# Kernel optimization log

Measured on AMD Instinct MI355X. Metric: run time of the kernel, lower is better.

The kernel has to match this reference:

```python
import jax, jax.numpy as jnp
import numpy as np

V, C, D = 4, 64, 64
LH, LW, FH, FW = 64, 96, 256, 384
MIN_DEPTH, MAX_DEPTH, MIN_UNC = 0.5, 10.0, 0.01


def conv2d(x, w, b=None, groups=1, pad=0):
    y = jax.lax.conv_general_dilated(x, w, (1, 1), [(pad, pad), (pad, pad)],
                                     feature_group_count=groups,
                                     dimension_numbers=('NCHW', 'OIHW', 'NCHW'))
    return y if b is None else y + b[None, :, None, None]


def group_norm(x, g, b, groups=8, eps=1e-5):
    N, Ch, H, W = x.shape
    xr = x.reshape(N, groups, Ch // groups, H, W)
    m = xr.mean((2, 3, 4), keepdims=True)
    v = ((xr - m) ** 2).mean((2, 3, 4), keepdims=True)
    xr = (xr - m) / jnp.sqrt(v + eps)
    return xr.reshape(N, Ch, H, W) * g[None, :, None, None] + b[None, :, None, None]


def ds_block(x, dw, pw_w, pw_b, gn_g, gn_b):
    # in_channels == out_channels everywhere here -> identity skip
    y = conv2d(x, dw, None, groups=x.shape[1], pad=1)
    y = conv2d(y, pw_w, pw_b)
    y = jax.nn.gelu(group_norm(y, gn_g, gn_b), approximate=False)
    return y + x


def resize_bilinear(x, oh, ow):
    # bilinear, align_corners=True, x: [N,C,H,W]
    N, Ch, H, W = x.shape
    ys = jnp.linspace(0.0, H - 1.0, oh)
    xs = jnp.linspace(0.0, W - 1.0, ow)
    y0 = jnp.clip(jnp.floor(ys).astype(jnp.int32), 0, H - 1)
    x0 = jnp.clip(jnp.floor(xs).astype(jnp.int32), 0, W - 1)
    y1 = jnp.minimum(y0 + 1, H - 1)
    x1 = jnp.minimum(x0 + 1, W - 1)
    wy = (ys - y0)[None, None, :, None]
    wx = (xs - x0)[None, None, None, :]
    r0 = x[:, :, y0, :]
    r1 = x[:, :, y1, :]
    a = r0[:, :, :, x0]; b = r0[:, :, :, x1]
    c = r1[:, :, :, x0]; d = r1[:, :, :, x1]
    return a * (1 - wy) * (1 - wx) + b * (1 - wy) * wx + c * wy * (1 - wx) + d * wy * wx


def grid_sample(img, grid):
    # bilinear, padding_mode='zeros', align_corners=True
    B, Ch, H, W = img.shape
    gx = (grid[..., 0] + 1.0) * 0.5 * (W - 1)
    gy = (grid[..., 1] + 1.0) * 0.5 * (H - 1)
    x0f = jnp.floor(gx); y0f = jnp.floor(gy)
    wx = gx - x0f; wy = gy - y0f
    def gather(xf, yf):
        valid = (xf >= 0) & (xf <= W - 1) & (yf >= 0) & (yf <= H - 1)
        xi = jnp.clip(xf, 0, W - 1).astype(jnp.int32)
        yi = jnp.clip(yf, 0, H - 1).astype(jnp.int32)
        v = jax.vmap(lambda im, yy, xx: im[:, yy, xx])(img, yi, xi)  # [B,C,Hg,Wg]
        return v * valid.astype(img.dtype)[:, None]
    return (gather(x0f, y0f) * ((1 - wx) * (1 - wy))[:, None]
            + gather(x0f + 1, y0f) * (wx * (1 - wy))[:, None]
            + gather(x0f, y0f + 1) * ((1 - wx) * wy)[:, None]
            + gather(x0f + 1, y0f + 1) * (wx * wy)[:, None])


def warp_volume(src_feats, inv_bins, K_ref, E_ref, K_src, W2C_src, H, W):
    # src_feats [B,C,H,W]; K_ref [3,3]; E_ref [4,4]; K_src [B,3,3]; W2C_src [B,4,4]
    B, Ch = src_feats.shape[:2]
    Dn = inv_bins.shape[0]
    depth_bins = 1.0 / inv_bins
    scale = jnp.array([W, H, 1.0], src_feats.dtype)
    Kr = K_ref * scale[:, None]
    Ks = K_src * scale[None, :, None]
    gy, gx = jnp.meshgrid(jnp.arange(H, dtype=src_feats.dtype),
                          jnp.arange(W, dtype=src_feats.dtype), indexing='ij')
    homog = jnp.stack([gx, gy, jnp.ones_like(gx)], 0).reshape(3, -1)          # [3,N]
    rays = jnp.linalg.inv(Kr) @ homog                                          # [3,N]
    ref_pts = rays[:, None, :] * depth_bins[None, :, None]                     # [3,D,N]
    world = jnp.einsum('ij,jdn->idn', E_ref[:3, :3], ref_pts) + E_ref[:3, 3][:, None, None]
    spts = jnp.einsum('bij,jdn->bidn', W2C_src[:, :3, :3], world) + W2C_src[:, :3, 3][:, :, None, None]
    proj = jnp.einsum('bij,bjdn->bidn', Ks, spts)                              # [B,3,D,N]
    xy = proj[:, :2] / jnp.maximum(proj[:, 2:3], 1e-6)
    xy = xy.reshape(B, 2, Dn, H, W)
    gxn = 2.0 * xy[:, 0] / max(W - 1, 1) - 1.0
    gyn = 2.0 * xy[:, 1] / max(H - 1, 1) - 1.0
    grid = jnp.stack([gxn, gyn], -1).reshape(B, Dn * H, W, 2)
    sz = proj[:, 2].reshape(B, Dn, H, W)
    vis = ((sz > 1e-6) & (xy[:, 0] >= 0) & (xy[:, 0] <= W - 1)
           & (xy[:, 1] >= 0) & (xy[:, 1] <= H - 1)).astype(src_feats.dtype)
    warped = grid_sample(src_feats, grid).reshape(B, Ch, Dn, H, W) * vis[:, None]
    return warped, vis


def _forward(lowres_features, fullres_features, images, intrinsics, extrinsics,
             dp_w, dp_b, cr_dw, cr_pw_w, cr_pw_b, cr_gn_g, cr_gn_b,
             fr_conv_w, fr_conv_b, fr_dw, fr_pw_w, fr_pw_b, fr_gn_g, fr_gn_b,
             res_w, res_b, conf_w, conf_b):
    nv, _, lh, lw = lowres_features.shape
    fh, fw = fullres_features.shape[-2:]
    imgs_r = resize_bilinear(images, fh, fw)
    inv_bins = jnp.linspace(1.0 / MAX_DEPTH, 1.0 / MIN_DEPTH, D).astype(lowres_features.dtype)
    w2c = jnp.linalg.inv(extrinsics)
    interval = (1.0 / MIN_DEPTH - 1.0 / MAX_DEPTH) / max(D - 1, 1)
    bins4 = inv_bins[None, :, None, None]
    depths, uncs, confs = [], [], []
    for r in range(nv):
        sidx = np.array([i for i in range(nv) if i != r])
        ref_feat = lowres_features[r]                       # [C,lh,lw]
        warped, vis = warp_volume(lowres_features[sidx], inv_bins,
                                  intrinsics[r], extrinsics[r],
                                  intrinsics[sidx], w2c[sidx], lh, lw)
        dot = jnp.einsum('chw,bcdhw->bdhw', ref_feat, warped)
        nr = jnp.sqrt((ref_feat ** 2).sum(0))               # [h,w]
        nw = jnp.sqrt((warped ** 2).sum(1))                 # [b,d,h,w]
        cos = dot / (jnp.maximum(nr, 1e-8) * jnp.maximum(nw, 1e-8))
        cost = (1.0 - cos) * vis + (1.0 - vis)
        agg = ((cost * vis).sum(0) / jnp.maximum(vis.sum(0), 1.0))[None]  # [1,D,h,w]
        rc = agg
        for i in range(2):
            rc = ds_block(rc, cr_dw[i], cr_pw_w[i], cr_pw_b[i], cr_gn_g[i], cr_gn_b[i])
        refined_cost = agg + rc
        logits = conv2d(ref_feat[None], dp_w, dp_b) - refined_cost
        prob = jax.nn.softmax(logits, axis=1)
        inv_low = (prob * bins4).sum(1, keepdims=True)
        var = (prob * (bins4 - inv_low) ** 2).sum(1, keepdims=True)
        inv_unc_low = jnp.maximum(jnp.sqrt(var), 1e-6)
        pdf_max = prob.max(axis=1, keepdims=True)
        inv_full = resize_bilinear(inv_low, fh, fw)
        inv_unc_full = resize_bilinear(inv_unc_low, fh, fw)
        pdf_max_full = resize_bilinear(pdf_max, fh, fw)
        y = jax.nn.gelu(conv2d(jnp.concatenate([fullres_features[r:r + 1], imgs_r[r:r + 1]], 1),
                               fr_conv_w, fr_conv_b, pad=1), approximate=False)
        for i in range(2):
            y = ds_block(y, fr_dw[i], fr_pw_w[i], fr_pw_b[i], fr_gn_g[i], fr_gn_b[i])
        resid = jnp.tanh(conv2d(y, res_w, res_b)) * interval
        inv_depth = jnp.clip(inv_full + resid, 1.0 / MAX_DEPTH, 1.0 / MIN_DEPTH)
        depth = 1.0 / inv_depth
        unc = jnp.maximum(inv_unc_full / jnp.maximum(inv_depth ** 2, 1e-6), MIN_UNC)
        conf = jax.nn.sigmoid(conv2d(y, conf_w, conf_b)) * pdf_max_full / (1.0 + inv_unc_full / max(interval, 1e-6))
        depths.append(depth); uncs.append(unc); confs.append(conf)
    return (jnp.concatenate(depths, 0), jnp.concatenate(uncs, 0), jnp.concatenate(confs, 0))


def setup_inputs() -> dict:
    key = jax.random.key(0)
    ks = jax.random.split(key, 16)
    f = jnp.float32
    lowres_features = jax.random.normal(ks[0], (V, C, LH, LW), f)
    fullres_features = jax.random.normal(ks[1], (V, C, FH, FW), f)
    images = jax.random.uniform(ks[2], (V, 3, FH, FW), dtype=f)
    # normalized pinhole intrinsics (module scales rows by width/height)
    K = np.array([[0.8, 0.0, 0.5], [0.0, 0.8, 0.5], [0.0, 0.0, 1.0]], np.float32)
    intrinsics = jnp.asarray(np.tile(K[None], (V, 1, 1)))
    # camera-to-world extrinsics: small y-rotations, 0.2m baseline steps
    angles = [0.0, 0.05, -0.05, 0.1]
    ext = np.tile(np.eye(4, dtype=np.float32)[None], (V, 1, 1))
    for v in range(V):
        a = angles[v]
        ext[v, :3, :3] = np.array([[np.cos(a), 0, np.sin(a)], [0, 1, 0], [-np.sin(a), 0, np.cos(a)]], np.float32)
        ext[v, 0, 3] = 0.2 * v
    extrinsics = jnp.asarray(ext)
    n = jax.random.normal
    return dict(
        lowres_features=lowres_features, fullres_features=fullres_features,
        images=images, intrinsics=intrinsics, extrinsics=extrinsics,
        dp_w=0.05 * n(ks[3], (D, C, 1, 1), f), dp_b=jnp.zeros((D,), f),
        cr_dw=0.1 * n(ks[4], (2, D, 1, 3, 3), f), cr_pw_w=0.05 * n(ks[5], (2, D, D, 1, 1), f),
        cr_pw_b=jnp.zeros((2, D), f), cr_gn_g=jnp.ones((2, D), f), cr_gn_b=jnp.zeros((2, D), f),
        fr_conv_w=0.05 * n(ks[6], (C, C + 3, 3, 3), f), fr_conv_b=jnp.zeros((C,), f),
        fr_dw=0.1 * n(ks[7], (2, C, 1, 3, 3), f), fr_pw_w=0.05 * n(ks[8], (2, C, C, 1, 1), f),
        fr_pw_b=jnp.zeros((2, C), f), fr_gn_g=jnp.ones((2, C), f), fr_gn_b=jnp.zeros((2, C), f),
        res_w=0.05 * n(ks[9], (1, C, 1, 1), f), res_b=jnp.zeros((1,), f),
        conf_w=0.05 * n(ks[10], (1, C, 1, 1), f), conf_b=jnp.zeros((1,), f))


def reference(lowres_features, fullres_features, images, intrinsics, extrinsics,
              dp_w, dp_b, cr_dw, cr_pw_w, cr_pw_b, cr_gn_g, cr_gn_b,
              fr_conv_w, fr_conv_b, fr_dw, fr_pw_w, fr_pw_b, fr_gn_g, fr_gn_b,
              res_w, res_b, conf_w, conf_b):
    return _forward(lowres_features, fullres_features, images, intrinsics, extrinsics,
                    dp_w, dp_b, cr_dw, cr_pw_w, cr_pw_b, cr_gn_g, cr_gn_b,
                    fr_conv_w, fr_conv_b, fr_dw, fr_pw_w, fr_pw_b, fr_gn_g, fr_gn_b,
                    res_w, res_b, conf_w, conf_b)
```

## Files before the change

kernel.cpp:

```cpp
#include <hip/hip_runtime.h>
#include <math.h>

#define DEV __device__ __forceinline__

namespace {

typedef short s8v __attribute__((ext_vector_type(8)));
typedef float f4v __attribute__((ext_vector_type(4)));

constexpr int V = 4, C = 64, D = 64;
constexpr int LH = 64, LW = 96, FH = 256, FW = 384;
constexpr int LNPX = LH * LW;
constexpr int FNPX = FH * FW;
constexpr float INTERVAL = 1.9f / 63.0f;

DEV float gelu_f(float x) { return 0.5f * x * (1.0f + erff(x * 0.70710678118654752f)); }
DEV unsigned short f2bf(float f) {
  unsigned int u = __float_as_uint(f);
  u += 0x7FFFu + ((u >> 16) & 1u);
  return (unsigned short)(u >> 16);
}
DEV float bfl(unsigned int u) { return __uint_as_float(u << 16); }
DEV float bfh(unsigned int u) { return __uint_as_float(u & 0xffff0000u); }
DEV float bfu(unsigned short s) { return __uint_as_float((unsigned int)s << 16); }

DEV void mm3(const float* a, const float* b, float* o) {
#pragma unroll
  for (int i = 0; i < 3; ++i)
#pragma unroll
    for (int j = 0; j < 3; ++j)
      o[i * 3 + j] = a[i * 3] * b[j] + a[i * 3 + 1] * b[3 + j] + a[i * 3 + 2] * b[6 + j];
}

DEV void inv3(const float* m, float* o) {
  float c00 = m[4] * m[8] - m[5] * m[7];
  float c01 = m[5] * m[6] - m[3] * m[8];
  float c02 = m[3] * m[7] - m[4] * m[6];
  float det = m[0] * c00 + m[1] * c01 + m[2] * c02;
  float id = 1.0f / det;
  o[0] = c00 * id; o[1] = (m[2] * m[7] - m[1] * m[8]) * id; o[2] = (m[1] * m[5] - m[2] * m[4]) * id;
  o[3] = c01 * id; o[4] = (m[0] * m[8] - m[2] * m[6]) * id; o[5] = (m[2] * m[3] - m[0] * m[5]) * id;
  o[6] = c02 * id; o[7] = (m[1] * m[6] - m[0] * m[7]) * id; o[8] = (m[0] * m[4] - m[1] * m[3]) * id;
}

DEV void inv4(const float* m, float* o) {
  float a[4][8];
  for (int i = 0; i < 4; ++i)
    for (int j = 0; j < 4; ++j) { a[i][j] = m[i * 4 + j]; a[i][j + 4] = (i == j) ? 1.0f : 0.0f; }
  for (int col = 0; col < 4; ++col) {
    int p = col;
    for (int r2 = col + 1; r2 < 4; ++r2)
      if (fabsf(a[r2][col]) > fabsf(a[p][col])) p = r2;
    if (p != col)
      for (int j = 0; j < 8; ++j) { float tt = a[col][j]; a[col][j] = a[p][j]; a[p][j] = tt; }
    float inv = 1.0f / a[col][col];
    for (int j = 0; j < 8; ++j) a[col][j] *= inv;
    for (int r2 = 0; r2 < 4; ++r2) {
      if (r2 == col) continue;
      float f = a[r2][col];
      for (int j = 0; j < 8; ++j) a[r2][j] -= f * a[col][j];
    }
  }
  for (int i = 0; i < 4; ++i)
    for (int j = 0; j < 4; ++j) o[i * 4 + j] = a[i][j + 4];
}

__global__ void k_setup(const float* __restrict__ intr, const float* __restrict__ ext,
                        float* __restrict__ mats) {
  int tid = threadIdx.x;
  if (tid >= 12) return;
  int r = tid / 3, s = tid % 3;
  int sv = s + (s >= r ? 1 : 0);
  const float scale[3] = {(float)LW, (float)LH, 1.0f};
  float Kr[9], Kri[9], Ks[9];
  for (int i = 0; i < 3; ++i)
    for (int j = 0; j < 3; ++j) {
      Kr[i * 3 + j] = intr[r * 9 + i * 3 + j] * scale[i];
      Ks[i * 3 + j] = intr[sv * 9 + i * 3 + j] * scale[i];
    }
  inv3(Kr, Kri);
  float Einv[16];
  inv4(ext + sv * 16, Einv);
  const float* Er = ext + r * 16;
  float A[9];
  for (int i = 0; i < 3; ++i)
    for (int j = 0; j < 3; ++j)
      A[i * 3 + j] = Einv[i * 4 + 0] * Er[0 * 4 + j] + Einv[i * 4 + 1] * Er[1 * 4 + j] +
                     Einv[i * 4 + 2] * Er[2 * 4 + j];
  float B[9], M[9];
  mm3(Ks, A, B);
  mm3(B, Kri, M);
  float bb[3];
  for (int i = 0; i < 3; ++i)
    bb[i] = Einv[i * 4 + 0] * Er[3] + Einv[i * 4 + 1] * Er[7] + Einv[i * 4 + 2] * Er[11] +
            Einv[i * 4 + 3];
  float t3[3];
  for (int i = 0; i < 3; ++i)
    t3[i] = Ks[i * 3 + 0] * bb[0] + Ks[i * 3 + 1] * bb[1] + Ks[i * 3 + 2] * bb[2];
  float* dst = mats + tid * 12;
  for (int k = 0; k < 9; ++k) dst[k] = M[k];
  for (int i = 0; i < 3; ++i) dst[9 + i] = t3[i];
}

__global__ void k_nr(const float* __restrict__ lr, float* __restrict__ nr) {
  int idx = blockIdx.x * 256 + threadIdx.x;
  int v = idx / LNPX, hw = idx % LNPX;
  const float* p = lr + (size_t)v * C * LNPX + hw;
  float s = 0.0f;
#pragma unroll 8
  for (int c = 0; c < C; ++c) { float f = p[c * LNPX]; s += f * f; }
  nr[idx] = sqrtf(s);
}

__global__ __launch_bounds__(256) void k_cost(const float* __restrict__ lr,
                                              const float* __restrict__ mats,
                                              const float* __restrict__ nr,
                                              float* __restrict__ agg) {
  int idx = blockIdx.x * 256 + threadIdx.x;
  int hw = idx % LNPX;
  int vd = idx / LNPX;
  int d = vd & 63;
  int r = vd >> 6;
  int h = hw / LW, w = hw - h * LW;
  float invb = 0.1f + d * INTERVAL;
  float depth = 1.0f / invb;
  float nrv = fmaxf(nr[r * LNPX + hw], 1e-8f);
  float fx = (float)w, fy = (float)h;
  int offs[3][4];
  float wts[3][4];
  float viss[3];
  const float* bases[3];
#pragma unroll
  for (int s = 0; s < 3; ++s) {
    int sv = s + (s >= r ? 1 : 0);
    const float* Mt = mats + (r * 3 + s) * 12;
    float px = depth * (Mt[0] * fx + Mt[1] * fy + Mt[2]) + Mt[9];
    float py = depth * (Mt[3] * fx + Mt[4] * fy + Mt[5]) + Mt[10];
    float pz = depth * (Mt[6] * fx + Mt[7] * fy + Mt[8]) + Mt[11];
    float iz = 1.0f / fmaxf(pz, 1e-6f);
    float gx = px * iz, gy = py * iz;
    bool vs = (pz > 1e-6f) && (gx >= 0.0f) && (gx <= (float)(LW - 1)) && (gy >= 0.0f) &&
              (gy <= (float)(LH - 1));
    viss[s] = vs ? 1.0f : 0.0f;
    float x0f = floorf(gx), y0f = floorf(gy);
    float wx = gx - x0f, wy = gy - y0f;
    int x0 = (int)x0f, y0 = (int)y0f;
#pragma unroll
    for (int ty = 0; ty < 2; ++ty)
#pragma unroll
      for (int tx = 0; tx < 2; ++tx) {
        int xx = x0 + tx, yy = y0 + ty;
        bool tv = vs && (xx >= 0) && (xx < LW) && (yy >= 0) && (yy < LH);
        offs[s][ty * 2 + tx] = tv ? (yy * LW + xx) : 0;
        float ww = (ty ? wy : 1.0f - wy) * (tx ? wx : 1.0f - wx);
        wts[s][ty * 2 + tx] = tv ? ww : 0.0f;
      }
    bases[s] = lr + (size_t)sv * C * LNPX;
  }
  float dots[3] = {0.f, 0.f, 0.f}, nws[3] = {0.f, 0.f, 0.f};
  const float* rp = lr + (size_t)r * C * LNPX + hw;
#pragma unroll 4
  for (int c = 0; c < C; ++c) {
    float rf = rp[c * LNPX];
#pragma unroll
    for (int s = 0; s < 3; ++s) {
      const float* p = bases[s] + c * LNPX;
      float wv = wts[s][0] * p[offs[s][0]] + wts[s][1] * p[offs[s][1]] +
                 wts[s][2] * p[offs[s][2]] + wts[s][3] * p[offs[s][3]];
      dots[s] += rf * wv;
      nws[s] += wv * wv;
    }
  }
  float csum = 0.0f, vsum = 0.0f;
#pragma unroll
  for (int s = 0; s < 3; ++s) {
    if (viss[s] > 0.0f) {
      float cosv = dots[s] / (nrv * fmaxf(sqrtf(nws[s]), 1e-8f));
      csum += 1.0f - cosv;
      vsum += 1.0f;
    }
  }
  agg[idx] = csum / fmaxf(vsum, 1.0f);
}

__global__ void k_dw(const float* __restrict__ in, float* __restrict__ out,
                     const float* __restrict__ wdw, int Hh, int Ww, int total) {
  int idx = blockIdx.x * 256 + threadIdx.x;
  if (idx >= total) return;
  int npx = Hh * Ww;
  int px = idx % npx;
  int vc = idx / npx;
  int c = vc & 63;
  int py = px / Ww, pxx = px - py * Ww;
  const float* wp = wdw + c * 9;
  const float* ip = in + (size_t)vc * npx;
  float acc = 0.0f;
#pragma unroll
  for (int ky = 0; ky < 3; ++ky) {
    int yy = py + ky - 1;
    if (yy < 0 || yy >= Hh) continue;
#pragma unroll
    for (int kx = 0; kx < 3; ++kx) {
      int xx = pxx + kx - 1;
      if (xx < 0 || xx >= Ww) continue;
      acc += wp[ky * 3 + kx] * ip[yy * Ww + xx];
    }
  }
  out[idx] = acc;
}

__global__ __launch_bounds__(256) void k_pw(float* buf, const float* __restrict__ wmat,
                                            const float* __restrict__ bias,
                                            double* __restrict__ stats, int npx) {
  __shared__ __align__(16) float s_in[64 * 68];
  __shared__ __align__(16) float s_w[64 * 68];
  int t = threadIdx.x;
  int v = blockIdx.y;
  int px0 = blockIdx.x * 64;
  float* base = buf + (size_t)v * 64 * npx;
#pragma unroll
  for (int rep = 0; rep < 16; ++rep) {
    int lin = rep * 256 + t;
    int hi = lin >> 6, lo = lin & 63;
    s_in[hi * 68 + lo] = base[(size_t)hi * npx + px0 + lo];
    s_w[lo * 68 + hi] = wmat[hi * 64 + lo];
  }
  __syncthreads();
  int pxb = (t & 15) * 4;
  int ocb = (t >> 4) * 4;
  float acc[4][4] = {{0.f}};
#pragma unroll 8
  for (int ic = 0; ic < 64; ++ic) {
    float4 a = *(const float4*)&s_in[ic * 68 + pxb];
    float4 wv = *(const float4*)&s_w[ic * 68 + ocb];
    acc[0][0] += wv.x * a.x; acc[0][1] += wv.x * a.y; acc[0][2] += wv.x * a.z; acc[0][3] += wv.x * a.w;
    acc[1][0] += wv.y * a.x; acc[1][1] += wv.y * a.y; acc[1][2] += wv.y * a.z; acc[1][3] += wv.y * a.w;
    acc[2][0] += wv.z * a.x; acc[2][1] += wv.z * a.y; acc[2][2] += wv.z * a.z; acc[2][3] += wv.z * a.w;
    acc[3][0] += wv.w * a.x; acc[3][1] += wv.w * a.y; acc[3][2] += wv.w * a.z; acc[3][3] += wv.w * a.w;
  }
  float s1 = 0.0f, s2 = 0.0f;
#pragma unroll
  for (int i = 0; i < 4; ++i) {
    float b = bias[ocb + i];
    float4 o;
    o.x = acc[i][0] + b; o.y = acc[i][1] + b; o.z = acc[i][2] + b; o.w = acc[i][3] + b;
    s1 += o.x + o.y + o.z + o.w;
    s2 += o.x * o.x + o.y * o.y + o.z * o.z + o.w * o.w;
    *(float4*)&base[(size_t)(ocb + i) * npx + px0 + pxb] = o;
  }
  __syncthreads();
  float* red = s_in;
  red[t] = s1;
  red[256 + t] = s2;
  __syncthreads();
  if (t < 8) {
    float a1 = 0.0f, a2 = 0.0f;
    for (int k = 0; k < 32; ++k) { a1 += red[t * 32 + k]; a2 += red[256 + t * 32 + k]; }
    atomicAdd(&stats[((size_t)v * 8 + t) * 2], (double)a1);
    atomicAdd(&stats[((size_t)v * 8 + t) * 2 + 1], (double)a2);
  }
}

__global__ void k_gn_apply(const float* __restrict__ xin, const float* res, float* out,
                           const double* __restrict__ stats, const float* __restrict__ gam,
                           const float* __restrict__ bet, int npx, int total) {
  int idx = blockIdx.x * 256 + threadIdx.x;
  if (idx >= total) return;
  int vc = idx / npx;
  int c = vc & 63;
  int v = vc >> 6;
  int g = c >> 3;
  float cntf = 8.0f * (float)npx;
  float s1 = (float)stats[((size_t)v * 8 + g) * 2];
  float s2 = (float)stats[((size_t)v * 8 + g) * 2 + 1];
  float mean = s1 / cntf;
  float var = s2 / cntf - mean * mean;
  float istd = rsqrtf(var + 1e-5f);
  float xn = (xin[idx] - mean) * istd * gam[c] + bet[c];
  out[idx] = gelu_f(xn) + res[idx];
}

__global__ __launch_bounds__(256) void k_dwpw(const float* __restrict__ x,
                                              float* __restrict__ tout,
                                              const float* __restrict__ wdw,
                                              const float* __restrict__ wpw,
                                              const float* __restrict__ bias,
                                              double* __restrict__ stats, int H, int W) {
  __shared__ __align__(16) unsigned short s_x[340 * 72];
  __shared__ __align__(16) unsigned short s_w[64 * 64];
  __shared__ __align__(16) float s_dww[9 * 64];
  int t = threadIdx.x, v = blockIdx.y;
  int ntx = W >> 5;
  int txw = (blockIdx.x % ntx) * 32, tyh = (blockIdx.x / ntx) * 8;
  int npx = H * W;
  const float* xb = x + (size_t)v * 64 * npx;
  for (int lin = t; lin < 340 * 32; lin += 256) {
    int px = lin % 340, pr = lin / 340;
    int ys = px / 34, xs = px - ys * 34;
    int gy = tyh + ys - 1, gx = txw + xs - 1;
    float v0 = 0.f, v1 = 0.f;
    if (gy >= 0 && gy < H && gx >= 0 && gx < W) {
      size_t o = (size_t)gy * W + gx;
      v0 = xb[(size_t)(2 * pr) * npx + o];
      v1 = xb[(size_t)(2 * pr + 1) * npx + o];
    }
    ((unsigned int*)s_x)[px * 36 + pr] =
        (unsigned int)f2bf(v0) | ((unsigned int)f2bf(v1) << 16);
  }
  for (int lin = t; lin < 4096; lin += 256) {
    int ic = lin >> 6, oc = lin & 63;
    s_w[ic * 64 + oc] = f2bf(wpw[oc * 64 + ic]);
  }
  for (int lin = t; lin < 576; lin += 256) {
    int ic = lin % 64, tap = lin / 64;
    s_dww[tap * 64 + ic] = wdw[ic * 9 + tap];
  }
  __syncthreads();
  int py = t >> 5, pxx = t & 31;
  float dwa[64];
#pragma unroll
  for (int i = 0; i < 64; ++i) dwa[i] = 0.f;
#pragma unroll
  for (int ky = 0; ky < 3; ++ky)
#pragma unroll
    for (int kx = 0; kx < 3; ++kx) {
      int slot = (py + ky) * 34 + (pxx + kx);
      const uint4* xr = (const uint4*)(s_x + slot * 72);
      const float4* wr = (const float4*)(s_dww + (ky * 3 + kx) * 64);
#pragma unroll
      for (int q = 0; q < 8; ++q) {
        uint4 u = xr[q];
        float4 wa = wr[2 * q], wb = wr[2 * q + 1];
        dwa[8 * q + 0] += bfl(u.x) * wa.x;
        dwa[8 * q + 1] += bfh(u.x) * wa.y;
        dwa[8 * q + 2] += bfl(u.y) * wa.z;
        dwa[8 * q + 3] += bfh(u.y) * wa.w;
        dwa[8 * q + 4] += bfl(u.z) * wb.x;
        dwa[8 * q + 5] += bfh(u.z) * wb.y;
        dwa[8 * q + 6] += bfl(u.w) * wb.z;
        dwa[8 * q + 7] += bfh(u.w) * wb.w;
      }
    }
  size_t obase = (size_t)v * 64 * npx + (size_t)(tyh + py) * W + (txw + pxx);
  float s1g[8], s2g[8];
#pragma unroll
  for (int i = 0; i < 8; ++i) { s1g[i] = 0.f; s2g[i] = 0.f; }
#pragma unroll
  for (int ocB = 0; ocB < 4; ++ocB) {
    float acc[16];
#pragma unroll
    for (int j = 0; j < 16; ++j) acc[j] = bias[ocB * 16 + j];
#pragma unroll
    for (int ic = 0; ic < 64; ++ic) {
      float a = dwa[ic];
      const unsigned short* wrow = s_w + ic * 64 + ocB * 16;
#pragma unroll
      for (int j4 = 0; j4 < 4; ++j4) {
        ushort4 wv = *(const ushort4*)(wrow + j4 * 4);
        acc[j4 * 4 + 0] += a * bfu(wv.x);
        acc[j4 * 4 + 1] += a * bfu(wv.y);
        acc[j4 * 4 + 2] += a * bfu(wv.z);
        acc[j4 * 4 + 3] += a * bfu(wv.w);
      }
    }
#pragma unroll
    for (int j = 0; j < 16; ++j) {
      float val = acc[j];
      tout[obase + (size_t)(ocB * 16 + j) * npx] = val;
      int grp = (ocB * 16 + j) >> 3;
      s1g[grp] += val;
      s2g[grp] += val * val;
    }
  }
  __syncthreads();
  float* red = (float*)s_x;
#pragma unroll
  for (int k = 0; k < 16; ++k) {
    float val = (k < 8) ? s1g[k] : s2g[k - 8];
    for (int off = 32; off; off >>= 1) val += __shfl_down(val, off);
    if ((t & 63) == 0) red[(t >> 6) * 16 + k] = val;
  }
  __syncthreads();
  if (t < 16) {
    float s = red[t] + red[16 + t] + red[32 + t] + red[48 + t];
    int grp = t & 7, which = t >> 3;
    atomicAdd(&stats[((size_t)v * 8 + grp) * 2 + which], (double)s);
  }
}

__global__ void k_gn4(const float4* __restrict__ xin, const float4* __restrict__ res,
                      float4* __restrict__ out, const double* __restrict__ stats,
                      const float* __restrict__ gam, const float* __restrict__ bet, int npx,
                      int total4) {
  int i4 = blockIdx.x * 256 + threadIdx.x;
  if (i4 >= total4) return;
  int npx4 = npx >> 2;
  int vc = i4 / npx4;
  int c = vc & 63;
  int v = vc >> 6;
  int g = c >> 3;
  float cntf = 8.0f * (float)npx;
  float s1 = (float)stats[((size_t)v * 8 + g) * 2];
  float s2 = (float)stats[((size_t)v * 8 + g) * 2 + 1];
  float mean = s1 / cntf;
  float var = s2 / cntf - mean * mean;
  float istd = rsqrtf(var + 1e-5f);
  float ga = gam[c], be = bet[c];
  float4 a = xin[i4], r = res[i4];
  float4 o;
  o.x = gelu_f((a.x - mean) * istd * ga + be) + r.x;
  o.y = gelu_f((a.y - mean) * istd * ga + be) + r.y;
  o.z = gelu_f((a.z - mean) * istd * ga + be) + r.z;
  o.w = gelu_f((a.w - mean) * istd * ga + be) + r.w;
  out[i4] = o;
}

__global__ void k_logits(const float* __restrict__ lr, const float* __restrict__ dpw,
                         const float* __restrict__ dpb, const float* __restrict__ agg,
                         const float* __restrict__ rc, float* __restrict__ out) {
  int idx = blockIdx.x * 256 + threadIdx.x;
  int hw = idx % LNPX;
  int vd = idx / LNPX;
  int d = vd & 63;
  int v = vd >> 6;
  const float* rp = lr + (size_t)v * C * LNPX + hw;
  const float* wp = dpw + d * 64;
  float s = 0.0f;
#pragma unroll 8
  for (int c = 0; c < C; ++c) s += wp[c] * rp[c * LNPX];
  out[idx] = s + dpb[d] - (agg[idx] + rc[idx]);
}

__global__ void k_softmax(const float* __restrict__ logits, float* __restrict__ minv,
                          float* __restrict__ munc, float* __restrict__ mpdf) {
  int idx = blockIdx.x * 256 + threadIdx.x;
  int hw = idx % LNPX;
  int v = idx / LNPX;
  const float* lp = logits + (size_t)v * D * LNPX + hw;
  float mx = -1e30f;
  for (int d2 = 0; d2 < D; ++d2) mx = fmaxf(mx, lp[d2 * LNPX]);
  float Z = 0.0f, Sb = 0.0f;
  for (int d2 = 0; d2 < D; ++d2) {
    float e = expf(lp[d2 * LNPX] - mx);
    Z += e;
    Sb += e * (0.1f + d2 * INTERVAL);
  }
  float mean = Sb / Z;
  float Sv = 0.0f;
  for (int d2 = 0; d2 < D; ++d2) {
    float e = expf(lp[d2 * LNPX] - mx);
    float db = (0.1f + d2 * INTERVAL) - mean;
    Sv += e * db * db;
  }
  minv[idx] = mean;
  munc[idx] = fmaxf(sqrtf(Sv / Z), 1e-6f);
  mpdf[idx] = 1.0f / Z;
}

__global__ void k_wprep(const float* __restrict__ w, unsigned short* __restrict__ wp) {
  int idx = blockIdx.x * 256 + threadIdx.x;
  if (idx >= 55296) return;
  int b = idx & 7;
  int oc = (idx >> 3) & 63;
  int g = (idx >> 9) & 3;
  int r = idx >> 11;
  int k9 = r % 9;
  int c = r / 9;
  int ic = c * 32 + g * 8 + b;
  float val = (ic < 67) ? w[(oc * 67 + ic) * 9 + k9] : 0.0f;
  wp[((c * 9 + k9) * 4 + g) * 520 + oc * 8 + b] = f2bf(val);
}

__global__ __launch_bounds__(256) void k_conv0m(const float* __restrict__ ff,
                                                const float* __restrict__ img,
                                                const unsigned short* __restrict__ wb,
                                                const float* __restrict__ bias,
                                                float* __restrict__ out) {
  __shared__ __align__(16) unsigned short s_in[324 * 40];
  __shared__ __align__(16) unsigned short s_wt[9 * 4 * 520];
  int t = threadIdx.x, v = blockIdx.y;
  int tx0 = (blockIdx.x % 24) * 16;
  int ty0 = (blockIdx.x / 24) * 16;
  int lane = t & 63, m = lane & 15, g = lane >> 4;
  int wy = (t >> 6) * 4;
  const float* fbase = ff + (size_t)v * 64 * FNPX;
  const float* ibase = img + (size_t)v * 3 * FNPX;
  f4v acc[4][4];
#pragma unroll
  for (int f = 0; f < 4; ++f)
#pragma unroll
    for (int n = 0; n < 4; ++n) acc[f][n] = {0.f, 0.f, 0.f, 0.f};
  for (int c = 0; c < 3; ++c) {
    for (int lin = t; lin < 324 * 16; lin += 256) {
      int px = lin % 324, pr = lin / 324;
      int ys = px / 18, xs = px - ys * 18;
      int gy = ty0 + ys - 1, gx = tx0 + xs - 1;
      int ic0 = c * 32 + pr * 2;
      float v0 = 0.f, v1 = 0.f;
      if (gy >= 0 && gy < FH && gx >= 0 && gx < FW) {
        size_t o = (size_t)gy * FW + gx;
        if (ic0 < 64) v0 = fbase[(size_t)ic0 * FNPX + o];
        else if (ic0 < 67) v0 = ibase[(size_t)(ic0 - 64) * FNPX + o];
        if (ic0 + 1 < 64) v1 = fbase[(size_t)(ic0 + 1) * FNPX + o];
        else if (ic0 + 1 < 67) v1 = ibase[(size_t)(ic0 - 63) * FNPX + o];
      }
      ((unsigned int*)s_in)[px * 20 + pr] =
          (unsigned int)f2bf(v0) | ((unsigned int)f2bf(v1) << 16);
    }
    {
      const unsigned int* src = (const unsigned int*)(wb + (size_t)c * 18720);
      for (int lin = t; lin < 9360; lin += 256) ((unsigned int*)s_wt)[lin] = src[lin];
    }
    __syncthreads();
#pragma unroll 1
    for (int k9 = 0; k9 < 9; ++k9) {
      int ky = k9 / 3, kx = k9 - ky * 3;
      s8v a[4], b[4];
#pragma unroll
      for (int f = 0; f < 4; ++f) {
        int slot = (wy + f + ky) * 18 + (m + kx);
        a[f] = *(const s8v*)&s_in[slot * 40 + g * 8];
      }
      int wbase = (k9 * 4 + g) * 520 + m * 8;
#pragma unroll
      for (int n = 0; n < 4; ++n) b[n] = *(const s8v*)&s_wt[wbase + n * 128];
#pragma unroll
      for (int f = 0; f < 4; ++f)
#pragma unroll
        for (int n = 0; n < 4; ++n)
          acc[f][n] = __builtin_amdgcn_mfma_f32_16x16x32_bf16(a[f], b[n], acc[f][n], 0, 0, 0);
    }
    __syncthreads();
  }
#pragma unroll
  for (int f = 0; f < 4; ++f) {
    int gyy = ty0 + wy + f;
#pragma unroll
    for (int n = 0; n < 4; ++n) {
      int oc = n * 16 + m;
      float bv = bias[oc];
      float4 o;
      o.x = gelu_f(acc[f][n][0] + bv);
      o.y = gelu_f(acc[f][n][1] + bv);
      o.z = gelu_f(acc[f][n][2] + bv);
      o.w = gelu_f(acc[f][n][3] + bv);
      *(float4*)&out[((size_t)(v * 64 + oc)) * FNPX + (size_t)gyy * FW + tx0 + 4 * g] = o;
    }
  }
}

__global__ void k_epilogue(const float* __restrict__ y, const float* __restrict__ minv,
                           const float* __restrict__ munc, const float* __restrict__ mpdf,
                           const float* __restrict__ resw, const float* __restrict__ resb,
                           const float* __restrict__ confw, const float* __restrict__ confb,
                           float* __restrict__ out) {
  int idx = blockIdx.x * 256 + threadIdx.x;
  int px = idx % FNPX;
  int v = idx / FNPX;
  const float* yp = y + (size_t)v * 64 * FNPX + px;
  float sr = 0.0f, sc = 0.0f;
#pragma unroll 8
  for (int c2 = 0; c2 < C; ++c2) {
    float f = yp[(size_t)c2 * FNPX];
    sr += resw[c2] * f;
    sc += confw[c2] * f;
  }
  float resid = tanhf(sr + resb[0]) * INTERVAL;
  float sig = 1.0f / (1.0f + expf(-(sc + confb[0])));
  int py = px / FW, pxx = px - py * FW;
  float fy = py * (63.0f / 255.0f);
  float fx = pxx * (95.0f / 383.0f);
  int y0 = (int)floorf(fy); if (y0 > 63) y0 = 63; if (y0 < 0) y0 = 0;
  int x0 = (int)floorf(fx); if (x0 > 95) x0 = 95; if (x0 < 0) x0 = 0;
  int y1 = min(y0 + 1, 63), x1 = min(x0 + 1, 95);
  float wy = fy - (float)y0, wx = fx - (float)x0;
  const float* bi = minv + v * LNPX;
  const float* bu = munc + v * LNPX;
  const float* bp = mpdf + v * LNPX;
  int o00 = y0 * LW + x0, o01 = y0 * LW + x1, o10 = y1 * LW + x0, o11 = y1 * LW + x1;
  float w00 = (1 - wy) * (1 - wx), w01 = (1 - wy) * wx, w10 = wy * (1 - wx), w11 = wy * wx;
  float invf = w00 * bi[o00] + w01 * bi[o01] + w10 * bi[o10] + w11 * bi[o11];
  float uncf = w00 * bu[o00] + w01 * bu[o01] + w10 * bu[o10] + w11 * bu[o11];
  float pdff = w00 * bp[o00] + w01 * bp[o01] + w10 * bp[o10] + w11 * bp[o11];
  float invd = fminf(fmaxf(invf + resid, 0.1f), 2.0f);
  float depth = 1.0f / invd;
  float unc = fmaxf(uncf / fmaxf(invd * invd, 1e-6f), 0.01f);
  float conf = sig * pdff / (1.0f + uncf * (63.0f / 1.9f));
  out[idx] = depth;
  out[(size_t)V * FNPX + idx] = unc;
  out[(size_t)2 * V * FNPX + idx] = conf;
}

}

extern "C" void kernel_launch(void* const* d_in, const int* in_sizes, int n_in, void* d_out,
                              int out_size, void* d_ws, size_t ws_size, hipStream_t stream) {
  (void)in_sizes; (void)n_in; (void)out_size; (void)ws_size;
  const float* lr = (const float*)d_in[0];
  const float* ff = (const float*)d_in[1];
  const float* img = (const float*)d_in[2];
  const float* intr = (const float*)d_in[3];
  const float* ext = (const float*)d_in[4];
  const float* dp_w = (const float*)d_in[5];
  const float* dp_b = (const float*)d_in[6];
  const float* cr_dw = (const float*)d_in[7];
  const float* cr_pw_w = (const float*)d_in[8];
  const float* cr_pw_b = (const float*)d_in[9];
  const float* cr_gn_g = (const float*)d_in[10];
  const float* cr_gn_b = (const float*)d_in[11];
  const float* fr_conv_w = (const float*)d_in[12];
  const float* fr_conv_b = (const float*)d_in[13];
  const float* fr_dw = (const float*)d_in[14];
  const float* fr_pw_w = (const float*)d_in[15];
  const float* fr_pw_b = (const float*)d_in[16];
  const float* fr_gn_g = (const float*)d_in[17];
  const float* fr_gn_b = (const float*)d_in[18];
  const float* res_w = (const float*)d_in[19];
  const float* res_b = (const float*)d_in[20];
  const float* conf_w = (const float*)d_in[21];
  const float* conf_b = (const float*)d_in[22];
  float* out = (float*)d_out;

  char* ws = (char*)d_ws;
  size_t off = 0;
  auto alloc = [&](size_t bytes) -> void* {
    void* p = ws + off;
    off += (bytes + 255) & ~(size_t)255;
    return p;
  };
  float* FA = (float*)alloc((size_t)V * C * FNPX * 4);
  float* FB = (float*)alloc((size_t)V * C * FNPX * 4);
  float* AGG = (float*)alloc((size_t)V * D * LNPX * 4);
  float* LA = (float*)alloc((size_t)V * D * LNPX * 4);
  float* LB = (float*)alloc((size_t)V * D * LNPX * 4);
  float* NR = (float*)alloc((size_t)V * LNPX * 4);
  float* MINV = (float*)alloc((size_t)V * LNPX * 4);
  float* MUNC = (float*)alloc((size_t)V * LNPX * 4);
  float* MPDF = (float*)alloc((size_t)V * LNPX * 4);
  float* MATS = (float*)alloc(12 * 12 * 4);
  unsigned short* WPREP = (unsigned short*)alloc(3 * 9 * 4 * 520 * 2);
  double* STATS = (double*)alloc(4 * V * 8 * 2 * sizeof(double));

  hipMemsetAsync(STATS, 0, 4 * V * 8 * 2 * sizeof(double), stream);
  k_setup<<<1, 64, 0, stream>>>(intr, ext, MATS);
  k_wprep<<<216, 256, 0, stream>>>(fr_conv_w, WPREP);
  k_nr<<<(V * LNPX) / 256, 256, 0, stream>>>(lr, NR);
  k_cost<<<(V * D * LNPX) / 256, 256, 0, stream>>>(lr, MATS, NR, AGG);

  for (int i = 0; i < 2; ++i) {
    const float* x = (i == 0) ? AGG : LA;
    k_dw<<<(V * D * LNPX) / 256, 256, 0, stream>>>(x, LB, cr_dw + i * D * 9, LH, LW,
                                                   V * D * LNPX);
    k_pw<<<dim3(LNPX / 64, V), 256, 0, stream>>>(LB, cr_pw_w + i * D * D, cr_pw_b + i * D,
                                                 STATS + (size_t)i * V * 8 * 2, LNPX);
    k_gn_apply<<<(V * D * LNPX) / 256, 256, 0, stream>>>(
        LB, x, LA, STATS + (size_t)i * V * 8 * 2, cr_gn_g + i * D, cr_gn_b + i * D, LNPX,
        V * D * LNPX);
  }
  k_logits<<<(V * D * LNPX) / 256, 256, 0, stream>>>(lr, dp_w, dp_b, AGG, LA, LB);
  k_softmax<<<(V * LNPX) / 256, 256, 0, stream>>>(LB, MINV, MUNC, MPDF);

  k_conv0m<<<dim3(24 * 16, V), 256, 0, stream>>>(ff, img, WPREP, fr_conv_b, FA);
  for (int i = 0; i < 2; ++i) {
    k_dwpw<<<dim3((FW / 32) * (FH / 8), V), 256, 0, stream>>>(
        FA, FB, fr_dw + i * C * 9, fr_pw_w + i * C * C, fr_pw_b + i * C,
        STATS + (size_t)(2 + i) * V * 8 * 2, FH, FW);
    k_gn4<<<(V * C * FNPX / 4 + 255) / 256, 256, 0, stream>>>(
        (const float4*)FB, (const float4*)FA, (float4*)FA, STATS + (size_t)(2 + i) * V * 8 * 2,
        fr_gn_g + i * C, fr_gn_b + i * C, FNPX, V * C * FNPX / 4);
  }
  k_epilogue<<<(V * FNPX) / 256, 256, 0, stream>>>(FA, MINV, MUNC, MPDF, res_w, res_b, conf_w,
                                                   conf_b, out);
}
```

Baseline: 1.325 ms.

## Transpose lowres features to pixel-major layout for vectorized cost-volume gathers

Adds a shared-memory transpose kernel that rewrites the lowres features from channel-major to pixel-major (HWC) order. The cost-volume, norm and logits kernels then read each pixel's 64 channels as contiguous float4 loads, so each bilinear tap fetches whole cache lines instead of 64 scattered strided loads. The cost is an extra 6 MB buffer plus one transpose pass, and in k_logits adjacent threads now stride 256 bytes apart where they used to read coalesced.

```diff
diff --git a/kernel.cpp b/kernel.cpp
--- a/kernel.cpp
+++ b/kernel.cpp
@@ -102,17 +102,40 @@
   for (int i = 0; i < 3; ++i) dst[9 + i] = t3[i];
 }
 
-__global__ void k_nr(const float* __restrict__ lr, float* __restrict__ nr) {
+__global__ __launch_bounds__(256) void k_tr(const float* __restrict__ lr,
+                                            float* __restrict__ lrt) {
+  __shared__ float s[64][65];
+  int v = blockIdx.y;
+  int hw0 = blockIdx.x * 64;
+  int t = threadIdx.x;
+#pragma unroll
+  for (int rep = 0; rep < 16; ++rep) {
+    int lin = rep * 256 + t;
+    int c = lin >> 6, lo = lin & 63;
+    s[c][lo] = lr[((size_t)v * 64 + c) * LNPX + hw0 + lo];
+  }
+  __syncthreads();
+#pragma unroll
+  for (int rep = 0; rep < 16; ++rep) {
+    int lin = rep * 256 + t;
+    int hwl = lin >> 6, c = lin & 63;
+    lrt[((size_t)v * LNPX + hw0 + hwl) * 64 + c] = s[c][hwl];
+  }
+}
+
+__global__ void k_nr(const float* __restrict__ lrt, float* __restrict__ nr) {
   int idx = blockIdx.x * 256 + threadIdx.x;
-  int v = idx / LNPX, hw = idx % LNPX;
-  const float* p = lr + (size_t)v * C * LNPX + hw;
+  const float4* p = (const float4*)(lrt + (size_t)idx * 64);
   float s = 0.0f;
-#pragma unroll 8
-  for (int c = 0; c < C; ++c) { float f = p[c * LNPX]; s += f * f; }
+#pragma unroll
+  for (int cb = 0; cb < 16; ++cb) {
+    float4 a = p[cb];
+    s += a.x * a.x + a.y * a.y + a.z * a.z + a.w * a.w;
+  }
   nr[idx] = sqrtf(s);
 }
 
-__global__ __launch_bounds__(256) void k_cost(const float* __restrict__ lr,
+__global__ __launch_bounds__(256) void k_cost(const float* __restrict__ lrt,
                                               const float* __restrict__ mats,
                                               const float* __restrict__ nr,
                                               float* __restrict__ agg) {
@@ -129,7 +152,7 @@
   int offs[3][4];
   float wts[3][4];
   float viss[3];
-  const float* bases[3];
+  const float4* b4[3];
 #pragma unroll
   for (int s = 0; s < 3; ++s) {
     int sv = s + (s >= r ? 1 : 0);
@@ -151,24 +174,30 @@
       for (int tx = 0; tx < 2; ++tx) {
         int xx = x0 + tx, yy = y0 + ty;
         bool tv = vs && (xx >= 0) && (xx < LW) && (yy >= 0) && (yy < LH);
-        offs[s][ty * 2 + tx] = tv ? (yy * LW + xx) : 0;
+        offs[s][ty * 2 + tx] = tv ? (yy * LW + xx) * 16 : 0;
         float ww = (ty ? wy : 1.0f - wy) * (tx ? wx : 1.0f - wx);
         wts[s][ty * 2 + tx] = tv ? ww : 0.0f;
       }
-    bases[s] = lr + (size_t)sv * C * LNPX;
-  }
+    b4[s] = (const float4*)(lrt + (size_t)sv * LNPX * 64);
+  }
+  const float4* rp = (const float4*)(lrt + ((size_t)r * LNPX + hw) * 64);
   float dots[3] = {0.f, 0.f, 0.f}, nws[3] = {0.f, 0.f, 0.f};
-  const float* rp = lr + (size_t)r * C * LNPX + hw;
 #pragma unroll 4
-  for (int c = 0; c < C; ++c) {
-    float rf = rp[c * LNPX];
+  for (int cb = 0; cb < 16; ++cb) {
+    float4 rf = rp[cb];
 #pragma unroll
     for (int s = 0; s < 3; ++s) {
-      const float* p = bases[s] + c * LNPX;
-      float wv = wts[s][0] * p[offs[s][0]] + wts[s][1] * p[offs[s][1]] +
-                 wts[s][2] * p[offs[s][2]] + wts[s][3] * p[offs[s][3]];
-      dots[s] += rf * wv;
-      nws[s] += wv * wv;
+      float4 t0 = b4[s][offs[s][0] + cb];
+      float4 t1 = b4[s][offs[s][1] + cb];
+      float4 t2 = b4[s][offs[s][2] + cb];
+      float4 t3 = b4[s][offs[s][3] + cb];
+      float w0 = wts[s][0], w1 = wts[s][1], w2 = wts[s][2], w3 = wts[s][3];
+      float wvx = w0 * t0.x + w1 * t1.x + w2 * t2.x + w3 * t3.x;
+      float wvy = w0 * t0.y + w1 * t1.y + w2 * t2.y + w3 * t3.y;
+      float wvz = w0 * t0.z + w1 * t1.z + w2 * t2.z + w3 * t3.z;
+      float wvw = w0 * t0.w + w1 * t1.w + w2 * t2.w + w3 * t3.w;
+      dots[s] += rf.x * wvx + rf.y * wvy + rf.z * wvz + rf.w * wvw;
+      nws[s] += wvx * wvx + wvy * wvy + wvz * wvz + wvw * wvw;
     }
   }
   float csum = 0.0f, vsum = 0.0f;
@@ -415,7 +444,7 @@
   out[i4] = o;
 }
 
-__global__ void k_logits(const float* __restrict__ lr, const float* __restrict__ dpw,
+__global__ void k_logits(const float* __restrict__ lrt, const float* __restrict__ dpw,
                          const float* __restrict__ dpb, const float* __restrict__ agg,
                          const float* __restrict__ rc, float* __restrict__ out) {
   int idx = blockIdx.x * 256 + threadIdx.x;
@@ -423,11 +452,15 @@
   int vd = idx / LNPX;
   int d = vd & 63;
   int v = vd >> 6;
-  const float* rp = lr + (size_t)v * C * LNPX + hw;
-  const float* wp = dpw + d * 64;
+  const float4* rp = (const float4*)(lrt + ((size_t)v * LNPX + hw) * 64);
+  const float4* wp = (const float4*)(dpw + d * 64);
   float s = 0.0f;
-#pragma unroll 8
-  for (int c = 0; c < C; ++c) s += wp[c] * rp[c * LNPX];
+#pragma unroll
+  for (int cb = 0; cb < 16; ++cb) {
+    float4 a = rp[cb];
+    float4 w4 = wp[cb];
+    s += a.x * w4.x + a.y * w4.y + a.z * w4.z + a.w * w4.w;
+  }
   out[idx] = s + dpb[d] - (agg[idx] + rc[idx]);
 }
 
@@ -633,6 +666,7 @@
   float* AGG = (float*)alloc((size_t)V * D * LNPX * 4);
   float* LA = (float*)alloc((size_t)V * D * LNPX * 4);
   float* LB = (float*)alloc((size_t)V * D * LNPX * 4);
+  float* LRT = (float*)alloc((size_t)V * LNPX * 64 * 4);
   float* NR = (float*)alloc((size_t)V * LNPX * 4);
   float* MINV = (float*)alloc((size_t)V * LNPX * 4);
   float* MUNC = (float*)alloc((size_t)V * LNPX * 4);
@@ -644,8 +678,9 @@
   hipMemsetAsync(STATS, 0, 4 * V * 8 * 2 * sizeof(double), stream);
   k_setup<<<1, 64, 0, stream>>>(intr, ext, MATS);
   k_wprep<<<216, 256, 0, stream>>>(fr_conv_w, WPREP);
-  k_nr<<<(V * LNPX) / 256, 256, 0, stream>>>(lr, NR);
-  k_cost<<<(V * D * LNPX) / 256, 256, 0, stream>>>(lr, MATS, NR, AGG);
+  k_tr<<<dim3(LNPX / 64, V), 256, 0, stream>>>(lr, LRT);
+  k_nr<<<(V * LNPX) / 256, 256, 0, stream>>>(LRT, NR);
+  k_cost<<<(V * D * LNPX) / 256, 256, 0, stream>>>(LRT, MATS, NR, AGG);
 
   for (int i = 0; i < 2; ++i) {
     const float* x = (i == 0) ? AGG : LA;
@@ -657,7 +692,7 @@
         LB, x, LA, STATS + (size_t)i * V * 8 * 2, cr_gn_g + i * D, cr_gn_b + i * D, LNPX,
         V * D * LNPX);
   }
-  k_logits<<<(V * D * LNPX) / 256, 256, 0, stream>>>(lr, dp_w, dp_b, AGG, LA, LB);
+  k_logits<<<(V * D * LNPX) / 256, 256, 0, stream>>>(LRT, dp_w, dp_b, AGG, LA, LB);
   k_softmax<<<(V * LNPX) / 256, 256, 0, stream>>>(LB, MINV, MUNC, MPDF);
 
   k_conv0m<<<dim3(24 * 16, V), 256, 0, stream>>>(ff, img, WPREP, fr_conv_b, FA);
```

Measured after the change: 1.627 ms. 1.23x slower.

## Split cost-volume channel loop across four thread groups with shared-memory reduction

Applied to the files above, without the earlier changes.

The cost-volume kernel now assigns each pixel-depth pair to four threads, each handling 16 of the 64 channels, and combines partial dot products and norms through shared memory before computing the cosine cost. This shortens each thread's serial gather loop and raises memory-level parallelism for the scattered bilinear reads. In exchange, projection math is duplicated four times per output, a block barrier and shared-memory traffic are added, and three quarters of the threads idle during the final step.

```diff
diff --git a/kernel.cpp b/kernel.cpp
--- a/kernel.cpp
+++ b/kernel.cpp
@@ -116,15 +116,15 @@
                                               const float* __restrict__ mats,
                                               const float* __restrict__ nr,
                                               float* __restrict__ agg) {
-  int idx = blockIdx.x * 256 + threadIdx.x;
-  int hw = idx % LNPX;
-  int vd = idx / LNPX;
-  int d = vd & 63;
-  int r = vd >> 6;
+  __shared__ float s_red[4 * 64 * 7];
+  int t = threadIdx.x;
+  int hw_l = t & 63, q = t >> 6;
+  int vd = blockIdx.y;
+  int d = vd & 63, r = vd >> 6;
+  int hw = blockIdx.x * 64 + hw_l;
   int h = hw / LW, w = hw - h * LW;
   float invb = 0.1f + d * INTERVAL;
   float depth = 1.0f / invb;
-  float nrv = fmaxf(nr[r * LNPX + hw], 1e-8f);
   float fx = (float)w, fy = (float)h;
   int offs[3][4];
   float wts[3][4];
@@ -155,32 +155,44 @@
         float ww = (ty ? wy : 1.0f - wy) * (tx ? wx : 1.0f - wx);
         wts[s][ty * 2 + tx] = tv ? ww : 0.0f;
       }
-    bases[s] = lr + (size_t)sv * C * LNPX;
+    bases[s] = lr + (size_t)sv * C * LNPX + (size_t)(q * 16) * LNPX;
   }
   float dots[3] = {0.f, 0.f, 0.f}, nws[3] = {0.f, 0.f, 0.f};
-  const float* rp = lr + (size_t)r * C * LNPX + hw;
+  const float* rp = lr + (size_t)r * C * LNPX + (size_t)(q * 16) * LNPX + hw;
 #pragma unroll 4
-  for (int c = 0; c < C; ++c) {
-    float rf = rp[c * LNPX];
+  for (int ci = 0; ci < 16; ++ci) {
+    float rf = rp[ci * LNPX];
 #pragma unroll
     for (int s = 0; s < 3; ++s) {
-      const float* p = bases[s] + c * LNPX;
+      const float* p = bases[s] + (size_t)ci * LNPX;
       float wv = wts[s][0] * p[offs[s][0]] + wts[s][1] * p[offs[s][1]] +
                  wts[s][2] * p[offs[s][2]] + wts[s][3] * p[offs[s][3]];
       dots[s] += rf * wv;
       nws[s] += wv * wv;
     }
   }
-  float csum = 0.0f, vsum = 0.0f;
-#pragma unroll
-  for (int s = 0; s < 3; ++s) {
-    if (viss[s] > 0.0f) {
-      float cosv = dots[s] / (nrv * fmaxf(sqrtf(nws[s]), 1e-8f));
-      csum += 1.0f - cosv;
-      vsum += 1.0f;
-    }
-  }
-  agg[idx] = csum / fmaxf(vsum, 1.0f);
+  float* my = s_red + (q * 64 + hw_l) * 7;
+  my[0] = dots[0]; my[1] = dots[1]; my[2] = dots[2];
+  my[3] = nws[0];  my[4] = nws[1];  my[5] = nws[2];
+  __syncthreads();
+  if (q == 0) {
+    float a6[6];
+#pragma unroll
+    for (int k = 0; k < 6; ++k)
+      a6[k] = s_red[(0 * 64 + hw_l) * 7 + k] + s_red[(1 * 64 + hw_l) * 7 + k] +
+              s_red[(2 * 64 + hw_l) * 7 + k] + s_red[(3 * 64 + hw_l) * 7 + k];
+    float nrv = fmaxf(nr[r * LNPX + hw], 1e-8f);
+    float csum = 0.0f, vsum = 0.0f;
+#pragma unroll
+    for (int s = 0; s < 3; ++s) {
+      if (viss[s] > 0.0f) {
+        float cosv = a6[s] / (nrv * fmaxf(sqrtf(a6[3 + s]), 1e-8f));
+        csum += 1.0f - cosv;
+        vsum += 1.0f;
+      }
+    }
+    agg[(size_t)vd * LNPX + hw] = csum / fmaxf(vsum, 1.0f);
+  }
 }
 
 __global__ void k_dw(const float* __restrict__ in, float* __restrict__ out,
@@ -645,7 +657,7 @@
   k_setup<<<1, 64, 0, stream>>>(intr, ext, MATS);
   k_wprep<<<216, 256, 0, stream>>>(fr_conv_w, WPREP);
   k_nr<<<(V * LNPX) / 256, 256, 0, stream>>>(lr, NR);
-  k_cost<<<(V * D * LNPX) / 256, 256, 0, stream>>>(lr, MATS, NR, AGG);
+  k_cost<<<dim3(LNPX / 64, V * D), 256, 0, stream>>>(lr, MATS, NR, AGG);
 
   for (int i = 0; i < 2; ++i) {
     const float* x = (i == 0) ? AGG : LA;
```

New measurement: 1.357 ms. 1.02x slower.
